# Kernel tuning notes

Hardware: AMD Instinct MI355X
Metric: run time of the kernel (lower is better)

The kernel has to match this reference:

```python
import jax, jax.numpy as jnp
import numpy as np

T = 32            # num_tsteps
B = 8192          # batch_size
W_IN0, W_OUT0 = 36, 18
W_IN1, W_OUT1 = 18, 8
TILE0, TILE1 = 2, 1
BETA = (0.95, 0.95)
TH = (0.55, 0.25)
Q = 15000.0       # sephia mrr_Q
ER_DB = 20.0      # sephia extinction ratio
IL_DB = 0.0       # sephia insertion loss
SHIFT_PM = -250.0 # sephia resonance shift per unit spike
P_UNITY = 1e-4    # dbm_to_watt(-10): optical power per WDM channel at unit input


def _lif(inp, mem, beta, th):
    # snntorch Leaky, reset_mechanism='zero', reset_delay=True:
    # reset decided from incoming mem, membrane zeroed before leak+integrate.
    reset = (mem > th).astype(inp.dtype)
    mem_new = (beta * mem + inp) * (1.0 - reset)
    spk = (mem_new > th).astype(inp.dtype)
    return spk, mem_new


def _allpass(spk, wl_nm):
    # All-pass MRR modulator: spike shifts the ring resonance by SHIFT_PM.
    # Normalized detuning delta = shift / (FWHM/2), FWHM = lambda / Q.
    fwhm_pm = wl_nm * 1e3 / Q                      # [C]
    delta = (spk * SHIFT_PM) / (0.5 * fwhm_pm)     # [B, C]
    gamma = 10.0 ** (-ER_DB / 20.0)                # on-resonance amplitude (ER)
    il = 10.0 ** (-IL_DB / 20.0)                   # insertion loss factor
    return (il * (1j * delta + gamma) / (1j * delta + 1.0)).astype(jnp.complex64)


def setup_inputs() -> dict:
    key = jax.random.key(0)
    ks = jax.random.split(key, 6)
    return {
        "x_in": jax.random.uniform(ks[0], (T, B, W_IN0), jnp.float32),
        "W0": jax.random.uniform(ks[1], (TILE0, W_IN0 // TILE0, W_OUT0 * 2 // TILE0), jnp.float32),
        "d0": jax.random.normal(ks[2], (TILE0, W_OUT0 // TILE0), jnp.float32) * 5e3,
        "W1": jax.random.uniform(ks[3], (TILE1, W_IN1 // TILE1, W_OUT1 * 2 // TILE1), jnp.float32),
        "d1": jax.random.normal(ks[4], (TILE1, W_OUT1 // TILE1), jnp.float32) * 5e3,
        "peak_powers_dbm": jax.random.uniform(ks[5], (W_IN0,), jnp.float32, -15.0, -5.0),
    }


def reference(x_in, W0, d0, W1, d1, peak_powers_dbm):
    wl0 = 1550.0 + 0.8 * jnp.arange(W_OUT0, dtype=jnp.float32)   # MRR resonance wavelengths (nm)
    # sephia_inputs: sqrt(dbm_to_watt(P_dbm) * 1e6) field amplitude per channel
    amp0 = jnp.sqrt((10.0 ** (peak_powers_dbm[:W_OUT0] / 10.0) / 1000.0) * 1e6)
    S0 = W_OUT0 * 2 // TILE0   # 18 spatial channels after EO broadcast
    S1 = W_OUT1 * 2 // TILE1   # 16 spatial channels into layer 1

    def step(carry, x_t):
        mem0, mem1 = carry
        b = x_t.shape[0]
        # --- EO conversion + layer 0 MRR weight bank (power domain) ---
        p_in = x_t * P_UNITY                                     # [B, 36] optical power
        p0 = jnp.broadcast_to(p_in[:, :, None], (b, W_IN0, S0)).reshape(b, TILE0, W_IN0 // TILE0, S0)
        I0 = jnp.einsum('btws,tws->bts', p0, W0)                 # photocurrents [B,2,18]
        cur0 = ((I0[..., 0::2] - I0[..., 1::2]) * d0).reshape(b, W_OUT0)  # balanced PDs + Diagonal
        spk0, mem0 = _lif(cur0, mem0, BETA[0], TH[0])
        # --- SEPhIA all-pass MRR modulation of comb lines ---
        lo = _allpass(spk0, wl0) * amp0.astype(jnp.complex64)    # [B, 18] complex field
        pw0 = jnp.abs(lo) ** 2                                   # detected power == spike record
        # --- post-SEPhIA broadcast + layer 1 weight bank ---
        p1 = jnp.broadcast_to(pw0[:, :, None], (b, W_IN1, S1)).reshape(b, TILE1, W_IN1 // TILE1, S1)
        I1 = jnp.einsum('btws,tws->bts', p1, W1)                 # [B,1,16]
        cur1 = ((I1[..., 0::2] - I1[..., 1::2]) * d1).reshape(b, W_OUT1)
        spk1, mem1 = _lif(cur1, mem1, BETA[1], TH[1])
        return (mem0, mem1), (pw0, spk1, mem0, mem1)

    mem0 = jnp.zeros((x_in.shape[1], W_OUT0), x_in.dtype)
    mem1 = jnp.zeros((x_in.shape[1], W_OUT1), x_in.dtype)
    _, (spks0, spks1, mems0, mems1) = jax.lax.scan(step, (mem0, mem1), x_in)
    return spks0, spks1, mems0, mems1
```

## Files before the change

kernel.cpp:

```cpp
#include <hip/hip_runtime.h>


namespace {
constexpr int Tn = 32;
constexpr int Bn = 8192;
constexpr int O_PW = 0;
constexpr int O_S1 = Tn * Bn * 18;
constexpr int O_M0 = O_S1 + Tn * Bn * 8;
constexpr int O_M1 = O_M0 + Tn * Bn * 18;
}

__global__ __launch_bounds__(256, 1)
void oesnn_kernel(const float* __restrict__ x_in,
                  const float* __restrict__ W0g,
                  const float* __restrict__ d0g,
                  const float* __restrict__ W1g,
                  const float* __restrict__ d1g,
                  const float* __restrict__ peakg,
                  float* __restrict__ out)
{
    const int lt  = threadIdx.x & 63;
    const int tid = blockIdx.x * 256 + threadIdx.x;
    const int b   = tid >> 3;
    const int sub = tid & 7;
    const int tl  = sub >> 2;
    const int q   = sub & 3;
    const int j0  = (q == 0) ? 0 : (2 * q + 1);
    const int nj  = (q == 0) ? 3 : 2;

    float w0e[3][18], w0o[3][18], dd0[3], pon[3], poff[3];
    #pragma unroll
    for (int j = 0; j < 3; ++j) {
        const int jc = (j < nj) ? (j0 + j) : j0;
        dd0[j] = d0g[tl * 9 + jc];
        #pragma unroll
        for (int w = 0; w < 18; ++w) {
            const float2 p = *(const float2*)(W0g + ((tl * 18 + w) * 18 + 2 * jc));
            w0e[j][w] = p.x;
            w0o[j][w] = p.y;
        }
        const int c = tl * 9 + jc;
        const float wl    = 1550.0f + 0.8f * (float)c;
        const float halfw = 0.5f * (wl * 1e3f / 15000.0f);
        const float amp   = sqrtf((exp10f(peakg[c] / 10.0f) / 1000.0f) * 1e6f);
        {
            const float lr = 0.1f * amp;
            const float a  = sqrtf(lr * lr);
            poff[j] = a * a;
        }
        {
            const float delta = -250.0f / halfw;
            const float den = fmaf(delta, delta, 1.0f);
            const float qr  = fmaf(delta, delta, 0.1f) / den;
            const float qi  = (delta - 0.1f * delta) / den;
            const float lr = qr * amp, li = qi * amp;
            const float a  = sqrtf(fmaf(lr, lr, li * li));
            pon[j] = a * a;
        }
    }

    float w1e[18], w1o[18];
    #pragma unroll
    for (int w = 0; w < 18; ++w) {
        const float2 pp = *(const float2*)(W1g + w * 16 + 2 * sub);
        w1e[w] = pp.x;
        w1o[w] = pp.y;
    }
    const float dd1 = d1g[sub];

    float mem0[3] = {0.f, 0.f, 0.f};
    float mem1 = 0.f;

    const float* xp = x_in + (size_t)b * 36 + tl * 18;
    float* opw = out + O_PW + (size_t)b * 18 + tl * 9 + j0;
    float* om0 = out + O_M0 + (size_t)b * 18 + tl * 9 + j0;
    float* os1 = out + O_S1 + (size_t)b * 8 + sub;
    float* om1 = out + O_M1 + (size_t)b * 8 + sub;

    float2 xv[9];
    #pragma unroll
    for (int k = 0; k < 9; ++k) xv[k] = *(const float2*)(xp + 2 * k);

    const int basel = lt & ~7;

    #pragma unroll 1
    for (int t = 0; t < Tn; ++t) {
        float p[18];
        #pragma unroll
        for (int k = 0; k < 9; ++k) {
            p[2 * k]     = xv[k].x * 1e-4f;
            p[2 * k + 1] = xv[k].y * 1e-4f;
        }
        xp += Bn * 36;
        if (t < Tn - 1) {
            #pragma unroll
            for (int k = 0; k < 9; ++k) xv[k] = *(const float2*)(xp + 2 * k);
        }

        float pwv[3];
        #pragma unroll
        for (int j = 0; j < 3; ++j) {
            float se = 0.f, so = 0.f;
            #pragma unroll
            for (int w = 0; w < 18; ++w) {
                se = fmaf(p[w], w0e[j][w], se);
                so = fmaf(p[w], w0o[j][w], so);
            }
            const float c0 = (se - so) * dd0[j];
            const float m  = mem0[j];
            const float m2 = (m > 0.55f) ? 0.0f : fmaf(0.95f, m, c0);
            mem0[j] = m2;
            pwv[j]  = (m2 > 0.55f) ? pon[j] : poff[j];
        }

        #pragma unroll
        for (int j = 0; j < 3; ++j) {
            if (j < nj) {
                opw[j] = pwv[j];
                om0[j] = mem0[j];
            }
        }

        float pwall[18];
        #pragma unroll
        for (int c = 0; c < 18; ++c) {
            const int tlc = c / 9, jc2 = c % 9;
            const int qo  = (jc2 < 3) ? 0 : ((jc2 - 1) / 2);
            const int st  = (qo == 0) ? 0 : (2 * qo + 1);
            const int r   = jc2 - st;
            pwall[c] = __shfl(pwv[r], basel + tlc * 4 + qo, 64);
        }

        float i1e = 0.f, i1o = 0.f;
        #pragma unroll
        for (int w = 0; w < 18; ++w) {
            i1e = fmaf(pwall[w], w1e[w], i1e);
            i1o = fmaf(pwall[w], w1o[w], i1o);
        }

        const float c1 = (i1e - i1o) * dd1;
        const float m  = mem1;
        const float m2 = (m > 0.25f) ? 0.0f : fmaf(0.95f, m, c1);
        mem1 = m2;
        *os1 = (m2 > 0.25f) ? 1.0f : 0.0f;
        *om1 = m2;

        opw += Bn * 18;
        om0 += Bn * 18;
        os1 += Bn * 8;
        om1 += Bn * 8;
    }
}

extern "C" void kernel_launch(void* const* d_in, const int* in_sizes, int n_in,
                              void* d_out, int out_size, void* d_ws, size_t ws_size,
                              hipStream_t stream) {
    (void)in_sizes; (void)n_in; (void)out_size; (void)d_ws; (void)ws_size;
    const float* x  = (const float*)d_in[0];
    const float* W0 = (const float*)d_in[1];
    const float* d0 = (const float*)d_in[2];
    const float* W1 = (const float*)d_in[3];
    const float* d1 = (const float*)d_in[4];
    const float* pk = (const float*)d_in[5];
    float* out = (float*)d_out;

    dim3 grid(Bn * 8 / 256), block(256);
    hipLaunchKernelGGL(oesnn_kernel, grid, block, 0, stream,
                       x, W0, d0, W1, d1, pk, out);
}
```

Measured before the change: 117.1 us.

## Split each batch row across 16 lanes and stage weights through LDS

Each batch element is now handled by 16 threads instead of 8. Each thread owns one or two layer-0 channels and one half of a layer-1 output pair, and the even/odd layer-1 partial sums are combined with an xor shuffle. Weights are first staged into shared memory in a repacked layout and then read as float4 into registers. Launch bounds move to allow 2 blocks per CU and the grid doubles. The aim is more parallelism and lower register pressure per thread, at the cost of duplicated x loads, an extra shuffle, and divergent stores on lanes that own a second channel.

```diff
diff --git a/kernel.cpp b/kernel.cpp
--- a/kernel.cpp
+++ b/kernel.cpp
@@ -8,9 +8,11 @@
 constexpr int O_S1 = Tn * Bn * 18;
 constexpr int O_M0 = O_S1 + Tn * Bn * 8;
 constexpr int O_M1 = O_M0 + Tn * Bn * 18;
+constexpr int LDS_W1 = 648;
+constexpr int LDS_TOT = 648 + 16 * 20;
 }
 
-__global__ __launch_bounds__(256, 1)
+__global__ __launch_bounds__(256, 2)
 void oesnn_kernel(const float* __restrict__ x_in,
                   const float* __restrict__ W0g,
                   const float* __restrict__ d0g,
@@ -19,77 +21,96 @@
                   const float* __restrict__ peakg,
                   float* __restrict__ out)
 {
-    const int lt  = threadIdx.x & 63;
-    const int tid = blockIdx.x * 256 + threadIdx.x;
-    const int b   = tid >> 3;
-    const int sub = tid & 7;
-    const int tl  = sub >> 2;
-    const int q   = sub & 3;
-    const int j0  = (q == 0) ? 0 : (2 * q + 1);
-    const int nj  = (q == 0) ? 3 : 2;
-
-    float w0e[3][18], w0o[3][18], dd0[3], pon[3], poff[3];
-    #pragma unroll
-    for (int j = 0; j < 3; ++j) {
-        const int jc = (j < nj) ? (j0 + j) : j0;
-        dd0[j] = d0g[tl * 9 + jc];
-        #pragma unroll
-        for (int w = 0; w < 18; ++w) {
-            const float2 p = *(const float2*)(W0g + ((tl * 18 + w) * 18 + 2 * jc));
-            w0e[j][w] = p.x;
-            w0o[j][w] = p.y;
-        }
-        const int c = tl * 9 + jc;
-        const float wl    = 1550.0f + 0.8f * (float)c;
-        const float halfw = 0.5f * (wl * 1e3f / 15000.0f);
-        const float amp   = sqrtf((exp10f(peakg[c] / 10.0f) / 1000.0f) * 1e6f);
-        {
-            const float lr = 0.1f * amp;
-            const float a  = sqrtf(lr * lr);
-            poff[j] = a * a;
-        }
-        {
+    __shared__ float lds[LDS_TOT];
+
+    for (int idx = threadIdx.x; idx < LDS_TOT; idx += 256) {
+        float v;
+        if (idx < LDS_W1) {
+            const int c  = idx / 36, r = idx - c * 36;
+            const int tl = c / 9,  jc = c - tl * 9;
+            const int w  = r >> 1, par = r & 1;
+            v = W0g[(tl * 18 + w) * 18 + 2 * jc + par];
+        } else {
+            const int k = idx - LDS_W1;
+            const int s = k / 20, w = k - s * 20;
+            v = (w < 18) ? W1g[w * 16 + s] : 0.0f;
+        }
+        lds[idx] = v;
+    }
+    __syncthreads();
+
+    const int lt   = threadIdx.x & 63;
+    const int tid  = blockIdx.x * 256 + threadIdx.x;
+    const int b    = tid >> 4;
+    const int sub  = tid & 15;
+    const int tl   = sub >> 3;
+    const int q    = sub & 7;
+    const int cA   = tl * 9 + q;
+    const bool has2 = (q == 0);
+    const int cB   = has2 ? (tl * 9 + 8) : cA;
+
+    const float dd0A = d0g[cA];
+    const float dd0B = d0g[cB];
+    const float dd1  = d1g[sub >> 1];
+
+    float ponA, poffA, ponB, poffB;
+    {
+        #pragma unroll
+        for (int which = 0; which < 2; ++which) {
+            const int c = which ? cB : cA;
+            const float wl    = 1550.0f + 0.8f * (float)c;
+            const float halfw = 0.5f * (wl * 1e3f / 15000.0f);
+            const float amp   = sqrtf((exp10f(peakg[c] / 10.0f) / 1000.0f) * 1e6f);
+            const float lr0 = 0.1f * amp;
+            const float a0  = sqrtf(lr0 * lr0);
+            const float poff = a0 * a0;
             const float delta = -250.0f / halfw;
             const float den = fmaf(delta, delta, 1.0f);
             const float qr  = fmaf(delta, delta, 0.1f) / den;
             const float qi  = (delta - 0.1f * delta) / den;
             const float lr = qr * amp, li = qi * amp;
             const float a  = sqrtf(fmaf(lr, lr, li * li));
-            pon[j] = a * a;
-        }
-    }
-
-    float w1e[18], w1o[18];
+            const float pon = a * a;
+            if (which) { ponB = pon; poffB = poff; }
+            else       { ponA = pon; poffA = poff; }
+        }
+    }
+
+    float4 wA[9], wB[9];
     #pragma unroll
-    for (int w = 0; w < 18; ++w) {
-        const float2 pp = *(const float2*)(W1g + w * 16 + 2 * sub);
-        w1e[w] = pp.x;
-        w1o[w] = pp.y;
-    }
-    const float dd1 = d1g[sub];
-
-    float mem0[3] = {0.f, 0.f, 0.f};
-    float mem1 = 0.f;
-
+    for (int k = 0; k < 9; ++k) {
+        wA[k] = ((const float4*)(lds + cA * 36))[k];
+        wB[k] = ((const float4*)(lds + cB * 36))[k];
+    }
+    float4 w1a[4];
+    float2 w1b;
+    #pragma unroll
+    for (int k = 0; k < 4; ++k)
+        w1a[k] = ((const float4*)(lds + LDS_W1 + sub * 20))[k];
+    w1b = ((const float2*)(lds + LDS_W1 + sub * 20))[8];
+
+    float mA = 0.f, mB = 0.f, m1 = 0.f;
     const float* xp = x_in + (size_t)b * 36 + tl * 18;
-    float* opw = out + O_PW + (size_t)b * 18 + tl * 9 + j0;
-    float* om0 = out + O_M0 + (size_t)b * 18 + tl * 9 + j0;
-    float* os1 = out + O_S1 + (size_t)b * 8 + sub;
-    float* om1 = out + O_M1 + (size_t)b * 8 + sub;
+    float* opwA = out + O_PW + (size_t)b * 18 + cA;
+    float* om0A = out + O_M0 + (size_t)b * 18 + cA;
+    float* opwB = out + O_PW + (size_t)b * 18 + cB;
+    float* om0B = out + O_M0 + (size_t)b * 18 + cB;
+    float* os1  = out + O_S1 + (size_t)b * 8 + (sub >> 1);
+    float* om1  = out + O_M1 + (size_t)b * 8 + (sub >> 1);
 
     float2 xv[9];
     #pragma unroll
     for (int k = 0; k < 9; ++k) xv[k] = *(const float2*)(xp + 2 * k);
 
-    const int basel = lt & ~7;
+    const int basel = lt & ~15;
 
     #pragma unroll 1
     for (int t = 0; t < Tn; ++t) {
-        float p[18];
+        float px[18];
         #pragma unroll
         for (int k = 0; k < 9; ++k) {
-            p[2 * k]     = xv[k].x * 1e-4f;
-            p[2 * k + 1] = xv[k].y * 1e-4f;
+            px[2 * k]     = xv[k].x * 1e-4f;
+            px[2 * k + 1] = xv[k].y * 1e-4f;
         }
         xp += Bn * 36;
         if (t < Tn - 1) {
@@ -97,58 +118,69 @@
             for (int k = 0; k < 9; ++k) xv[k] = *(const float2*)(xp + 2 * k);
         }
 
-        float pwv[3];
-        #pragma unroll
-        for (int j = 0; j < 3; ++j) {
-            float se = 0.f, so = 0.f;
-            #pragma unroll
-            for (int w = 0; w < 18; ++w) {
-                se = fmaf(p[w], w0e[j][w], se);
-                so = fmaf(p[w], w0o[j][w], so);
-            }
-            const float c0 = (se - so) * dd0[j];
-            const float m  = mem0[j];
-            const float m2 = (m > 0.55f) ? 0.0f : fmaf(0.95f, m, c0);
-            mem0[j] = m2;
-            pwv[j]  = (m2 > 0.55f) ? pon[j] : poff[j];
-        }
-
-        #pragma unroll
-        for (int j = 0; j < 3; ++j) {
-            if (j < nj) {
-                opw[j] = pwv[j];
-                om0[j] = mem0[j];
-            }
+        float seA = 0.f, soA = 0.f, seB = 0.f, soB = 0.f;
+        #pragma unroll
+        for (int k = 0; k < 9; ++k) {
+            const float4 fa = wA[k];
+            seA = fmaf(px[2 * k],     fa.x, seA);
+            soA = fmaf(px[2 * k],     fa.y, soA);
+            seA = fmaf(px[2 * k + 1], fa.z, seA);
+            soA = fmaf(px[2 * k + 1], fa.w, soA);
+            const float4 fb = wB[k];
+            seB = fmaf(px[2 * k],     fb.x, seB);
+            soB = fmaf(px[2 * k],     fb.y, soB);
+            seB = fmaf(px[2 * k + 1], fb.z, seB);
+            soB = fmaf(px[2 * k + 1], fb.w, soB);
+        }
+        const float c0A = (seA - soA) * dd0A;
+        const float m2A = (mA > 0.55f) ? 0.0f : fmaf(0.95f, mA, c0A);
+        mA = m2A;
+        const float pwA = (m2A > 0.55f) ? ponA : poffA;
+
+        const float c0B = (seB - soB) * dd0B;
+        const float m2B = (mB > 0.55f) ? 0.0f : fmaf(0.95f, mB, c0B);
+        mB = m2B;
+        const float pwB = (m2B > 0.55f) ? ponB : poffB;
+
+        opwA[0] = pwA;
+        om0A[0] = m2A;
+        if (has2) {
+            opwB[0] = pwB;
+            om0B[0] = m2B;
         }
 
         float pwall[18];
         #pragma unroll
         for (int c = 0; c < 18; ++c) {
-            const int tlc = c / 9, jc2 = c % 9;
-            const int qo  = (jc2 < 3) ? 0 : ((jc2 - 1) / 2);
-            const int st  = (qo == 0) ? 0 : (2 * qo + 1);
-            const int r   = jc2 - st;
-            pwall[c] = __shfl(pwv[r], basel + tlc * 4 + qo, 64);
-        }
-
-        float i1e = 0.f, i1o = 0.f;
-        #pragma unroll
-        for (int w = 0; w < 18; ++w) {
-            i1e = fmaf(pwall[w], w1e[w], i1e);
-            i1o = fmaf(pwall[w], w1o[w], i1o);
-        }
-
-        const float c1 = (i1e - i1o) * dd1;
-        const float m  = mem1;
-        const float m2 = (m > 0.25f) ? 0.0f : fmaf(0.95f, m, c1);
-        mem1 = m2;
-        *os1 = (m2 > 0.25f) ? 1.0f : 0.0f;
-        *om1 = m2;
-
-        opw += Bn * 18;
-        om0 += Bn * 18;
-        os1 += Bn * 8;
-        om1 += Bn * 8;
+            const int tlc = c / 9, jc = c - 9 * tlc;
+            const int own = basel + tlc * 8 + ((jc == 8) ? 0 : jc);
+            pwall[c] = __shfl((jc == 8) ? pwB : pwA, own, 64);
+        }
+
+        float i1 = 0.f;
+        #pragma unroll
+        for (int k = 0; k < 4; ++k) {
+            const float4 f = w1a[k];
+            i1 = fmaf(pwall[4 * k],     f.x, i1);
+            i1 = fmaf(pwall[4 * k + 1], f.y, i1);
+            i1 = fmaf(pwall[4 * k + 2], f.z, i1);
+            i1 = fmaf(pwall[4 * k + 3], f.w, i1);
+        }
+        i1 = fmaf(pwall[16], w1b.x, i1);
+        i1 = fmaf(pwall[17], w1b.y, i1);
+
+        const float i1p = __shfl_xor(i1, 1, 64);
+        const float c1  = (i1 - i1p) * dd1;
+        const float m2  = (m1 > 0.25f) ? 0.0f : fmaf(0.95f, m1, c1);
+        m1 = m2;
+        if (!(sub & 1)) {
+            *os1 = (m2 > 0.25f) ? 1.0f : 0.0f;
+            *om1 = m2;
+        }
+
+        opwA += Bn * 18; om0A += Bn * 18;
+        opwB += Bn * 18; om0B += Bn * 18;
+        os1  += Bn * 8;  om1  += Bn * 8;
     }
 }
 
@@ -164,7 +196,7 @@
     const float* pk = (const float*)d_in[5];
     float* out = (float*)d_out;
 
-    dim3 grid(Bn * 8 / 256), block(256);
+    dim3 grid(Bn * 16 / 256), block(256);
     hipLaunchKernelGGL(oesnn_kernel, grid, block, 0, stream,
                        x, W0, d0, W1, d1, pk, out);
 }
```

Measured after the change: 122.8 us. +4.9%, slower.

## Map one batch row per wavefront with one output column per lane

Applied to the files above, without the earlier changes.

Each wavefront now handles a single batch element instead of eight threads per element. Lanes 0-35 each compute one layer-0 column: an even/odd partial dot product, combined with a shfl_xor to form the balanced photocurrent. Lanes 36-51 each compute one layer-1 column from 18 broadcast shuffles. This cuts per-thread registers from about 108 weights to 18 and raises the launch-bounds occupancy hint to 4. The cost is 8x more threads, with 12 of 64 lanes idle, and each lane reads x redundantly. Stores become narrow, scattered single floats per lane.

```diff
diff --git a/kernel.cpp b/kernel.cpp
--- a/kernel.cpp
+++ b/kernel.cpp
@@ -10,7 +10,7 @@
 constexpr int O_M1 = O_M0 + Tn * Bn * 18;
 }
 
-__global__ __launch_bounds__(256, 1)
+__global__ __launch_bounds__(256, 4)
 void oesnn_kernel(const float* __restrict__ x_in,
                   const float* __restrict__ W0g,
                   const float* __restrict__ d0g,
@@ -19,136 +19,101 @@
                   const float* __restrict__ peakg,
                   float* __restrict__ out)
 {
-    const int lt  = threadIdx.x & 63;
-    const int tid = blockIdx.x * 256 + threadIdx.x;
-    const int b   = tid >> 3;
-    const int sub = tid & 7;
-    const int tl  = sub >> 2;
-    const int q   = sub & 3;
-    const int j0  = (q == 0) ? 0 : (2 * q + 1);
-    const int nj  = (q == 0) ? 3 : 2;
+    const int lane = threadIdx.x & 63;
+    const int wv   = threadIdx.x >> 6;
+    const int b    = blockIdx.x * 4 + wv;
 
-    float w0e[3][18], w0o[3][18], dd0[3], pon[3], poff[3];
+    const bool isL0 = lane < 36;
+    const int  par  = lane & 1;
+    const int  c0i  = isL0 ? (lane >> 1) : 0;
+    const int  tl   = c0i / 9;
+    const int  jc   = c0i - 9 * tl;
+    const bool isL1 = (lane >= 36) && (lane < 52);
+    const int  col  = isL1 ? (lane - 36) : 0;
+    const int  o1   = col >> 1;
+
+    float wreg[18];
     #pragma unroll
-    for (int j = 0; j < 3; ++j) {
-        const int jc = (j < nj) ? (j0 + j) : j0;
-        dd0[j] = d0g[tl * 9 + jc];
-        #pragma unroll
-        for (int w = 0; w < 18; ++w) {
-            const float2 p = *(const float2*)(W0g + ((tl * 18 + w) * 18 + 2 * jc));
-            w0e[j][w] = p.x;
-            w0o[j][w] = p.y;
-        }
-        const int c = tl * 9 + jc;
+    for (int w = 0; w < 18; ++w)
+        wreg[w] = isL0 ? W0g[(tl * 18 + w) * 18 + 2 * jc + par]
+                       : W1g[w * 16 + col];
+    #pragma unroll
+    for (int w = 0; w < 18; ++w) { asm volatile("" : "+v"(wreg[w])); }
+
+    const float dd0 = d0g[c0i];
+    const float dd1 = d1g[o1];
+
+    float pon, poff;
+    {
+        const int   c     = c0i;
         const float wl    = 1550.0f + 0.8f * (float)c;
         const float halfw = 0.5f * (wl * 1e3f / 15000.0f);
         const float amp   = sqrtf((exp10f(peakg[c] / 10.0f) / 1000.0f) * 1e6f);
-        {
-            const float lr = 0.1f * amp;
-            const float a  = sqrtf(lr * lr);
-            poff[j] = a * a;
-        }
-        {
-            const float delta = -250.0f / halfw;
-            const float den = fmaf(delta, delta, 1.0f);
-            const float qr  = fmaf(delta, delta, 0.1f) / den;
-            const float qi  = (delta - 0.1f * delta) / den;
-            const float lr = qr * amp, li = qi * amp;
-            const float a  = sqrtf(fmaf(lr, lr, li * li));
-            pon[j] = a * a;
-        }
+        const float lr0   = 0.1f * amp;
+        const float a0    = sqrtf(lr0 * lr0);
+        poff = a0 * a0;
+        const float delta = -250.0f / halfw;
+        const float den   = fmaf(delta, delta, 1.0f);
+        const float qr    = fmaf(delta, delta, 0.1f) / den;
+        const float qi    = (delta - 0.1f * delta) / den;
+        const float lr = qr * amp, li = qi * amp;
+        const float a  = sqrtf(fmaf(lr, lr, li * li));
+        pon = a * a;
     }
 
-    float w1e[18], w1o[18];
-    #pragma unroll
-    for (int w = 0; w < 18; ++w) {
-        const float2 pp = *(const float2*)(W1g + w * 16 + 2 * sub);
-        w1e[w] = pp.x;
-        w1o[w] = pp.y;
-    }
-    const float dd1 = d1g[sub];
-
-    float mem0[3] = {0.f, 0.f, 0.f};
-    float mem1 = 0.f;
-
+    float mem0 = 0.f, mem1 = 0.f;
     const float* xp = x_in + (size_t)b * 36 + tl * 18;
-    float* opw = out + O_PW + (size_t)b * 18 + tl * 9 + j0;
-    float* om0 = out + O_M0 + (size_t)b * 18 + tl * 9 + j0;
-    float* os1 = out + O_S1 + (size_t)b * 8 + sub;
-    float* om1 = out + O_M1 + (size_t)b * 8 + sub;
+    float* opw = out + O_PW + (size_t)b * 18 + c0i;
+    float* om0 = out + O_M0 + (size_t)b * 18 + c0i;
+    float* os1 = out + O_S1 + (size_t)b * 8 + o1;
+    float* om1 = out + O_M1 + (size_t)b * 8 + o1;
 
     float2 xv[9];
     #pragma unroll
     for (int k = 0; k < 9; ++k) xv[k] = *(const float2*)(xp + 2 * k);
 
-    const int basel = lt & ~7;
-
     #pragma unroll 1
     for (int t = 0; t < Tn; ++t) {
-        float p[18];
+        float acc = 0.f;
         #pragma unroll
         for (int k = 0; k < 9; ++k) {
-            p[2 * k]     = xv[k].x * 1e-4f;
-            p[2 * k + 1] = xv[k].y * 1e-4f;
+            acc = fmaf(xv[k].x * 1e-4f, wreg[2 * k],     acc);
+            acc = fmaf(xv[k].y * 1e-4f, wreg[2 * k + 1], acc);
         }
+
         xp += Bn * 36;
         if (t < Tn - 1) {
             #pragma unroll
             for (int k = 0; k < 9; ++k) xv[k] = *(const float2*)(xp + 2 * k);
         }
 
-        float pwv[3];
-        #pragma unroll
-        for (int j = 0; j < 3; ++j) {
-            float se = 0.f, so = 0.f;
-            #pragma unroll
-            for (int w = 0; w < 18; ++w) {
-                se = fmaf(p[w], w0e[j][w], se);
-                so = fmaf(p[w], w0o[j][w], so);
-            }
-            const float c0 = (se - so) * dd0[j];
-            const float m  = mem0[j];
-            const float m2 = (m > 0.55f) ? 0.0f : fmaf(0.95f, m, c0);
-            mem0[j] = m2;
-            pwv[j]  = (m2 > 0.55f) ? pon[j] : poff[j];
+        const float accp = __shfl_xor(acc, 1, 64);
+        const float cc0  = (acc - accp) * dd0;
+        const float m2A  = (mem0 > 0.55f) ? 0.0f : fmaf(0.95f, mem0, cc0);
+        mem0 = m2A;
+        const float pw   = (m2A > 0.55f) ? pon : poff;
+        if (isL0 && !par) {
+            opw[0] = pw;
+            om0[0] = m2A;
         }
 
+        float i1 = 0.f;
         #pragma unroll
-        for (int j = 0; j < 3; ++j) {
-            if (j < nj) {
-                opw[j] = pwv[j];
-                om0[j] = mem0[j];
-            }
+        for (int c = 0; c < 18; ++c) {
+            const float pv = __shfl(pw, 2 * c, 64);
+            i1 = fmaf(pv, wreg[c], i1);
+        }
+        const float i1p = __shfl_xor(i1, 1, 64);
+        const float cc1 = (i1 - i1p) * dd1;
+        const float m2B = (mem1 > 0.25f) ? 0.0f : fmaf(0.95f, mem1, cc1);
+        mem1 = m2B;
+        if (isL1 && !par) {
+            os1[0] = (m2B > 0.25f) ? 1.0f : 0.0f;
+            om1[0] = m2B;
         }
 
-        float pwall[18];
-        #pragma unroll
-        for (int c = 0; c < 18; ++c) {
-            const int tlc = c / 9, jc2 = c % 9;
-            const int qo  = (jc2 < 3) ? 0 : ((jc2 - 1) / 2);
-            const int st  = (qo == 0) ? 0 : (2 * qo + 1);
-            const int r   = jc2 - st;
-            pwall[c] = __shfl(pwv[r], basel + tlc * 4 + qo, 64);
-        }
-
-        float i1e = 0.f, i1o = 0.f;
-        #pragma unroll
-        for (int w = 0; w < 18; ++w) {
-            i1e = fmaf(pwall[w], w1e[w], i1e);
-            i1o = fmaf(pwall[w], w1o[w], i1o);
-        }
-
-        const float c1 = (i1e - i1o) * dd1;
-        const float m  = mem1;
-        const float m2 = (m > 0.25f) ? 0.0f : fmaf(0.95f, m, c1);
-        mem1 = m2;
-        *os1 = (m2 > 0.25f) ? 1.0f : 0.0f;
-        *om1 = m2;
-
-        opw += Bn * 18;
-        om0 += Bn * 18;
-        os1 += Bn * 8;
-        om1 += Bn * 8;
+        opw += Bn * 18; om0 += Bn * 18;
+        os1 += Bn * 8;  om1 += Bn * 8;
     }
 }
 
@@ -164,7 +129,7 @@
     const float* pk = (const float*)d_in[5];
     float* out = (float*)d_out;
 
-    dim3 grid(Bn * 8 / 256), block(256);
+    dim3 grid(Bn / 4), block(256);
     hipLaunchKernelGGL(oesnn_kernel, grid, block, 0, stream,
                        x, W0, d0, W1, d1, pk, out);
 }
```

Result: slower. 167.8 us (+43.3%).
